# Performance work log

Measured on AMD Instinct MI355X. Metric: run time of the kernel, lower is better.

## Reference

```python
import jax, jax.numpy as jnp
import numpy as np

N_NODES = 100000
N_EDGES = 3200000
N_GRAPHS = 128
IN_DIM = 4
HID = 64
BN_EPS = 1e-5


def setup_inputs() -> dict:
    key = jax.random.key(0)
    ks = jax.random.split(key, 24)
    x = jax.random.normal(ks[0], (N_NODES, IN_DIM), dtype=jnp.float32)
    edge_index = jax.random.randint(ks[1], (2, N_EDGES), 0, N_NODES, dtype=jnp.int32)
    batch_ids = jnp.sort(jax.random.randint(ks[2], (N_NODES,), 0, N_GRAPHS, dtype=jnp.int32))

    def lin(k, out_d, in_d):
        s = 1.0 / np.sqrt(in_d)
        return jax.random.uniform(k, (out_d, in_d), jnp.float32, -s, s)

    inp = {
        'x': x, 'edge_index': edge_index, 'batch_ids': batch_ids,
        # SAGEConv i: out = lin_l(mean_neighbors) + lin_r(x_self); bias lives in lin_l
        'w1l': lin(ks[3], HID, IN_DIM), 'b1': jnp.zeros((HID,), jnp.float32), 'w1r': lin(ks[4], HID, IN_DIM),
        'bn1_g': jnp.ones((HID,), jnp.float32), 'bn1_b': jnp.zeros((HID,), jnp.float32),
        'w2l': lin(ks[5], HID, HID), 'b2': jnp.zeros((HID,), jnp.float32), 'w2r': lin(ks[6], HID, HID),
        'bn2_g': jnp.ones((HID,), jnp.float32), 'bn2_b': jnp.zeros((HID,), jnp.float32),
        'w3l': lin(ks[7], HID, HID), 'b3': jnp.zeros((HID,), jnp.float32), 'w3r': lin(ks[8], HID, HID),
        'bn3_g': jnp.ones((HID,), jnp.float32), 'bn3_b': jnp.zeros((HID,), jnp.float32),
        'fc1_w': lin(ks[9], 64, HID), 'fc1_b': jnp.zeros((64,), jnp.float32),
        'fc2_w': lin(ks[10], 2, 64), 'fc2_b': jnp.zeros((2,), jnp.float32),
    }
    return inp


def _sage(x, src, dst, deg_inv, wl, bl, wr):
    # mean-aggregate neighbor messages (source -> target), then two small GEMMs
    msum = jax.ops.segment_sum(x[src], dst, num_segments=N_NODES)  # [N, d]
    agg = msum * deg_inv[:, None]
    return agg @ wl.T + bl + x @ wr.T


def _bn(x, g, b):
    # BatchNorm1d in training mode: batch stats over node dim, biased variance
    m = jnp.mean(x, axis=0)
    v = jnp.mean((x - m) ** 2, axis=0)
    return (x - m) * jax.lax.rsqrt(v + BN_EPS) * g + b


def reference(x, edge_index, batch_ids,
              w1l, b1, w1r, bn1_g, bn1_b,
              w2l, b2, w2r, bn2_g, bn2_b,
              w3l, b3, w3r, bn3_g, bn3_b,
              fc1_w, fc1_b, fc2_w, fc2_b):
    src, dst = edge_index[0], edge_index[1]
    deg = jax.ops.segment_sum(jnp.ones((src.shape[0],), x.dtype), dst, num_segments=N_NODES)
    deg_inv = 1.0 / jnp.maximum(deg, 1.0)

    h = jax.nn.relu(_bn(_sage(x, src, dst, deg_inv, w1l, b1, w1r), bn1_g, bn1_b))
    h = jax.nn.relu(_bn(_sage(h, src, dst, deg_inv, w2l, b2, w2r), bn2_g, bn2_b))
    h = jax.nn.relu(_bn(_sage(h, src, dst, deg_inv, w3l, b3, w3r), bn3_g, bn3_b))

    # global_mean_pool over graphs
    gsum = jax.ops.segment_sum(h, batch_ids, num_segments=N_GRAPHS)
    gcnt = jax.ops.segment_sum(jnp.ones((h.shape[0],), h.dtype), batch_ids, num_segments=N_GRAPHS)
    pooled = gsum / jnp.maximum(gcnt, 1.0)[:, None]

    # MLP head (dropout = identity at inference)
    hid = jax.nn.relu(pooled @ fc1_w.T + fc1_b)
    return hid @ fc2_w.T + fc2_b
```

## Files before the change

### kernel.cpp

```cpp
#include <hip/hip_runtime.h>
#include <hip/hip_fp16.h>

#define NN 100000
#define NE 3200000
#define NG 128
#define BN_EPS 1e-5f

#define NBUK 782
#define BSHIFT 7
#define BCAP 6144

#define GRID_SG 1024
#define PBMAX 2048
#define PSLICE 8

typedef _Float16 h2v __attribute__((ext_vector_type(2)));
typedef unsigned int u32x2 __attribute__((ext_vector_type(2)));
typedef unsigned int u32x4 __attribute__((ext_vector_type(4)));


__global__ void __launch_bounds__(512) k_scatter(
    const int* __restrict__ src, const int* __restrict__ dst,
    int* __restrict__ slab_cursor, unsigned int* __restrict__ slab, int E) {
    __shared__ int hist[NBUK + 2];
    __shared__ int cbase[NBUK + 2];
    int tid = threadIdx.x;
    int eBeg = blockIdx.x * 6250;
    int eEnd = min(eBeg + 6250, E);

    for (int t = tid; t < NBUK; t += 512) hist[t] = 0;
    __syncthreads();
    for (int e = eBeg + tid; e < eEnd; e += 512) {
        int b = dst[e] >> BSHIFT;
        atomicAdd(&hist[b], 1);
    }
    __syncthreads();
    for (int t = tid; t < NBUK; t += 512) {
        int c = hist[t];
        cbase[t] = (c > 0) ? atomicAdd(&slab_cursor[t], c) : 0;
    }
    __syncthreads();
    for (int t = tid; t < NBUK; t += 512) hist[t] = 0;
    __syncthreads();
    for (int e = eBeg + tid; e < eEnd; e += 512) {
        int d = dst[e];
        int b = d >> BSHIFT;
        int r = atomicAdd(&hist[b], 1);
        int pos = cbase[b] + r;
        if (pos < BCAP) slab[(size_t)b * BCAP + pos] = ((unsigned)src[e] << BSHIFT) | (unsigned)(d & 127);
    }
}

__global__ void __launch_bounds__(512) k_bucket_csr(
    const unsigned int* __restrict__ slab, const int* __restrict__ slab_cursor,
    int* __restrict__ row_ptr,
    float* __restrict__ deg_inv, int* __restrict__ csr_src,
    const float* __restrict__ x, const float* __restrict__ w1l,
    const float* __restrict__ b1, const float* __restrict__ w1r,
    __half* __restrict__ hp16, float* __restrict__ part) {
    __shared__ int lds_csr[BCAP];
    __shared__ int red[512];
    __shared__ int sdeg[128];
    __shared__ int sscan[128];
    __shared__ int slcur[128];
    __shared__ float swl[256], swr[256], sb1[64];
    __shared__ float ssum[64], ssq[64];
    int tid = threadIdx.x;
    int b = blockIdx.x;
    int lo = b << BSHIFT;
    int cnt = min(slab_cursor[b], BCAP);
    const unsigned int* sl = slab + (size_t)b * BCAP;

    int partial = 0;
    for (int j = tid; j < b; j += 512) partial += min(slab_cursor[j], BCAP);
    red[tid] = partial;
    __syncthreads();
    for (int off = 256; off > 0; off >>= 1) {
        if (tid < off) red[tid] += red[tid + off];
        __syncthreads();
    }
    int base = red[0];
    if (b == NBUK - 1 && tid == 0) row_ptr[NN] = base + cnt;

    if (tid < 256) { swl[tid] = w1l[tid]; swr[tid] = w1r[tid]; }
    if (tid < 64)  { sb1[tid] = b1[tid]; ssum[tid] = 0.f; ssq[tid] = 0.f; }
    if (tid < 128) sdeg[tid] = 0;
    __syncthreads();
    for (int k = tid; k < cnt; k += 512) {
        atomicAdd(&sdeg[sl[k] & 127], 1);
    }
    __syncthreads();
    int v = (tid < 128) ? sdeg[tid] : 0;
    if (tid < 128) sscan[tid] = v;
    __syncthreads();
    for (int off = 1; off < 128; off <<= 1) {
        int add = 0;
        if (tid < 128 && tid >= off) add = sscan[tid - off];
        __syncthreads();
        if (tid < 128) sscan[tid] += add;
        __syncthreads();
    }
    if (tid < 128) {
        int excl = sscan[tid] - v;
        int n = lo + tid;
        if (n < NN) {
            row_ptr[n] = base + excl;
            deg_inv[n] = 1.0f / fmaxf((float)v, 1.0f);
        }
        slcur[tid] = excl;
    }
    __syncthreads();
    for (int k = tid; k < cnt; k += 512) {
        unsigned int p = sl[k];
        int pos = atomicAdd(&slcur[p & 127], 1);
        lds_csr[pos] = (int)(p >> BSHIFT);
    }
    __syncthreads();
    for (int k = tid; k < cnt; k += 512) csr_src[base + k] = lds_csr[k];

    int i = tid >> 2, c = tid & 3;
    int n = lo + i;
    bool valid = (n < NN);
    int dhi = sscan[i];
    int dlo = dhi - sdeg[i];
    const float4* x4 = (const float4*)x;
    float4 acc = make_float4(0.f, 0.f, 0.f, 0.f);
    int k = dlo + c;
    for (; k + 12 < dhi; k += 16) {
        int s0 = lds_csr[k], s1 = lds_csr[k + 4], s2 = lds_csr[k + 8], s3 = lds_csr[k + 12];
        float4 v0 = x4[s0];
        float4 v1 = x4[s1];
        float4 v2 = x4[s2];
        float4 v3 = x4[s3];
        acc.x += v0.x + v1.x + v2.x + v3.x;
        acc.y += v0.y + v1.y + v2.y + v3.y;
        acc.z += v0.z + v1.z + v2.z + v3.z;
        acc.w += v0.w + v1.w + v2.w + v3.w;
    }
    for (; k < dhi; k += 4) {
        int s = lds_csr[k];
        float4 xv = x4[s];
        acc.x += xv.x; acc.y += xv.y; acc.z += xv.z; acc.w += xv.w;
    }
#pragma unroll
    for (int m = 1; m <= 2; m <<= 1) {
        acc.x += __shfl_xor(acc.x, m);
        acc.y += __shfl_xor(acc.y, m);
        acc.z += __shfl_xor(acc.z, m);
        acc.w += __shfl_xor(acc.w, m);
    }
    float dv = 1.0f / fmaxf((float)sdeg[i], 1.0f);
    float ax = acc.x * dv, ay = acc.y * dv, az = acc.z * dv, aw = acc.w * dv;
    float4 xs = valid ? x4[n] : make_float4(0.f, 0.f, 0.f, 0.f);

#pragma unroll
    for (int m4 = 0; m4 < 4; m4++) {
        float4 o = make_float4(0.f, 0.f, 0.f, 0.f);
        float* op = &o.x;
        if (valid) {
#pragma unroll
            for (int t = 0; t < 4; t++) {
                int j = c * 16 + m4 * 4 + t;
                float s = sb1[j];
                s += ax * swl[j * 4 + 0] + ay * swl[j * 4 + 1] + az * swl[j * 4 + 2] + aw * swl[j * 4 + 3];
                s += xs.x * swr[j * 4 + 0] + xs.y * swr[j * 4 + 1] + xs.z * swr[j * 4 + 2] + xs.w * swr[j * 4 + 3];
                op[t] = s;
            }
            h2v p0 = h2v{(_Float16)o.x, (_Float16)o.y};
            h2v p1 = h2v{(_Float16)o.z, (_Float16)o.w};
            u32x2 w;
            w.x = *(unsigned int*)&p0;
            w.y = *(unsigned int*)&p1;
            __builtin_nontemporal_store(w, (u32x2*)hp16 + (size_t)n * 16 + c * 4 + m4);
        }
        float4 q = make_float4(o.x * o.x, o.y * o.y, o.z * o.z, o.w * o.w);
#pragma unroll
        for (int m = 4; m <= 32; m <<= 1) {
            o.x += __shfl_xor(o.x, m); o.y += __shfl_xor(o.y, m);
            o.z += __shfl_xor(o.z, m); o.w += __shfl_xor(o.w, m);
            q.x += __shfl_xor(q.x, m); q.y += __shfl_xor(q.y, m);
            q.z += __shfl_xor(q.z, m); q.w += __shfl_xor(q.w, m);
        }
        if ((tid & 63) < 4) {
            int jb = c * 16 + m4 * 4;
            atomicAdd(&ssum[jb + 0], o.x); atomicAdd(&ssum[jb + 1], o.y);
            atomicAdd(&ssum[jb + 2], o.z); atomicAdd(&ssum[jb + 3], o.w);
            atomicAdd(&ssq[jb + 0], q.x);  atomicAdd(&ssq[jb + 1], q.y);
            atomicAdd(&ssq[jb + 2], q.z);  atomicAdd(&ssq[jb + 3], q.w);
        }
    }
    __syncthreads();
    if (tid < 64) {
        part[(2 * tid) * PBMAX + blockIdx.x]     = ssum[tid];
        part[(2 * tid + 1) * PBMAX + blockIdx.x] = ssq[tid];
    }
}

__global__ void __launch_bounds__(512, 8) k_sage(
    const __half* __restrict__ h_in, const float* __restrict__ sbv_in,
    const int* __restrict__ row_ptr,
    const int* __restrict__ csr_src, const float* __restrict__ deg_inv,
    const float* __restrict__ wl, const float* __restrict__ bl,
    const float* __restrict__ wr, __half* __restrict__ hp16,
    float* __restrict__ part) {
    __shared__ h2v wl2s[32][68];
    __shared__ h2v wr2s[32][68];
    __shared__ h2v tAh[32][36];
    __shared__ h2v tXh[32][36];
    __shared__ float ssum[64], ssq[64];
    int tid = threadIdx.x;
    for (int idx = tid; idx < 2048; idx += 512) {
        int j = idx & 63, kk = idx >> 6;
        float2 l = ((const float2*)wl)[j * 32 + kk];
        float2 r = ((const float2*)wr)[j * 32 + kk];
        wl2s[kk][j] = h2v{(_Float16)l.x, (_Float16)l.y};
        wr2s[kk][j] = h2v{(_Float16)r.x, (_Float16)r.y};
    }
    if (tid < 64) { ssum[tid] = 0.f; ssq[tid] = 0.f; }
    __syncthreads();

    int g = tid & 15, ni = tid >> 4;
    h2v sch0 = h2v{(_Float16)sbv_in[4 * g + 0], (_Float16)sbv_in[4 * g + 1]};
    h2v sch1 = h2v{(_Float16)sbv_in[4 * g + 2], (_Float16)sbv_in[4 * g + 3]};
    h2v bih0 = h2v{(_Float16)sbv_in[64 + 4 * g + 0], (_Float16)sbv_in[64 + 4 * g + 1]};
    h2v bih1 = h2v{(_Float16)sbv_in[64 + 4 * g + 2], (_Float16)sbv_in[64 + 4 * g + 3]};
    h2v hz = h2v{(_Float16)0.f, (_Float16)0.f};

    const uint2* tbl = (const uint2*)h_in;
    const int ntiles = NN / 32;

#define BN_ACC(vv) { \
        h2v a0 = *(h2v*)&vv.x, a1 = *(h2v*)&vv.y; \
        a0 = __builtin_elementwise_max(a0 * sch0 + bih0, hz); \
        a1 = __builtin_elementwise_max(a1 * sch1 + bih1, hz); \
        ax += (float)a0.x; ay += (float)a0.y; az += (float)a1.x; aw += (float)a1.y; }

    for (int tile = blockIdx.x; tile < ntiles; tile += GRID_SG) {
        int n = tile * 32 + ni;
        float ax = 0.f, ay = 0.f, az = 0.f, aw = 0.f;
        int r0 = row_ptr[n], r1 = row_ptr[n + 1];
        int e = r0;
        for (; e + 8 <= r1; e += 8) {
            int s0 = csr_src[e],     s1 = csr_src[e + 1], s2 = csr_src[e + 2], s3 = csr_src[e + 3];
            int s4 = csr_src[e + 4], s5 = csr_src[e + 5], s6 = csr_src[e + 6], s7 = csr_src[e + 7];
            uint2 v0 = tbl[(size_t)s0 * 16 + g];
            uint2 v1 = tbl[(size_t)s1 * 16 + g];
            uint2 v2 = tbl[(size_t)s2 * 16 + g];
            uint2 v3 = tbl[(size_t)s3 * 16 + g];
            uint2 v4 = tbl[(size_t)s4 * 16 + g];
            uint2 v5 = tbl[(size_t)s5 * 16 + g];
            uint2 v6 = tbl[(size_t)s6 * 16 + g];
            uint2 v7 = tbl[(size_t)s7 * 16 + g];
            BN_ACC(v0) BN_ACC(v1) BN_ACC(v2) BN_ACC(v3)
            BN_ACC(v4) BN_ACC(v5) BN_ACC(v6) BN_ACC(v7)
        }
        for (; e < r1; ++e) {
            int s = csr_src[e];
            uint2 vv = tbl[(size_t)s * 16 + g];
            BN_ACC(vv)
        }
        float di = deg_inv[n];
        uint2 rsv = tbl[(size_t)n * 16 + g];
        h2v xs0h = __builtin_elementwise_max(*(h2v*)&rsv.x * sch0 + bih0, hz);
        h2v xs1h = __builtin_elementwise_max(*(h2v*)&rsv.y * sch1 + bih1, hz);
        ax *= di; ay *= di; az *= di; aw *= di;
        tAh[ni][2 * g]     = h2v{(_Float16)ax, (_Float16)ay};
        tAh[ni][2 * g + 1] = h2v{(_Float16)az, (_Float16)aw};
        tXh[ni][2 * g]     = xs0h;
        tXh[ni][2 * g + 1] = xs1h;
        __syncthreads();

        float4 o = ((const float4*)bl)[g];
#pragma unroll 4
        for (int kk = 0; kk < 32; kk++) {
            h2v a2 = tAh[ni][kk];
            h2v x2 = tXh[ni][kk];
            h2v l0 = wl2s[kk][4 * g + 0], l1 = wl2s[kk][4 * g + 1];
            h2v l2 = wl2s[kk][4 * g + 2], l3 = wl2s[kk][4 * g + 3];
            h2v r0v = wr2s[kk][4 * g + 0], r1v = wr2s[kk][4 * g + 1];
            h2v r2v = wr2s[kk][4 * g + 2], r3v = wr2s[kk][4 * g + 3];
#if __has_builtin(__builtin_amdgcn_fdot2)
            o.x = __builtin_amdgcn_fdot2(a2, l0, o.x, false);
            o.y = __builtin_amdgcn_fdot2(a2, l1, o.y, false);
            o.z = __builtin_amdgcn_fdot2(a2, l2, o.z, false);
            o.w = __builtin_amdgcn_fdot2(a2, l3, o.w, false);
            o.x = __builtin_amdgcn_fdot2(x2, r0v, o.x, false);
            o.y = __builtin_amdgcn_fdot2(x2, r1v, o.y, false);
            o.z = __builtin_amdgcn_fdot2(x2, r2v, o.z, false);
            o.w = __builtin_amdgcn_fdot2(x2, r3v, o.w, false);
#else
            float b0 = (float)a2.x, b1 = (float)a2.y, x0 = (float)x2.x, x1 = (float)x2.y;
            o.x += b0 * (float)l0.x + b1 * (float)l0.y + x0 * (float)r0v.x + x1 * (float)r0v.y;
            o.y += b0 * (float)l1.x + b1 * (float)l1.y + x0 * (float)r1v.x + x1 * (float)r1v.y;
            o.z += b0 * (float)l2.x + b1 * (float)l2.y + x0 * (float)r2v.x + x1 * (float)r2v.y;
            o.w += b0 * (float)l3.x + b1 * (float)l3.y + x0 * (float)r3v.x + x1 * (float)r3v.y;
#endif
        }
        {
            h2v p0 = h2v{(_Float16)o.x, (_Float16)o.y};
            h2v p1 = h2v{(_Float16)o.z, (_Float16)o.w};
            u32x2 w;
            w.x = *(unsigned int*)&p0;
            w.y = *(unsigned int*)&p1;
            __builtin_nontemporal_store(w, (u32x2*)hp16 + (size_t)n * 16 + g);
        }

        float4 qv = make_float4(o.x * o.x, o.y * o.y, o.z * o.z, o.w * o.w);
#pragma unroll
        for (int m = 16; m <= 32; m <<= 1) {
            o.x += __shfl_xor(o.x, m); o.y += __shfl_xor(o.y, m);
            o.z += __shfl_xor(o.z, m); o.w += __shfl_xor(o.w, m);
            qv.x += __shfl_xor(qv.x, m); qv.y += __shfl_xor(qv.y, m);
            qv.z += __shfl_xor(qv.z, m); qv.w += __shfl_xor(qv.w, m);
        }
        if ((tid & 48) == 0) {
            atomicAdd(&ssum[4 * g + 0], o.x); atomicAdd(&ssum[4 * g + 1], o.y);
            atomicAdd(&ssum[4 * g + 2], o.z); atomicAdd(&ssum[4 * g + 3], o.w);
            atomicAdd(&ssq[4 * g + 0], qv.x);  atomicAdd(&ssq[4 * g + 1], qv.y);
            atomicAdd(&ssq[4 * g + 2], qv.z);  atomicAdd(&ssq[4 * g + 3], qv.w);
        }
        __syncthreads();
    }
#undef BN_ACC
    if (tid < 64) {
        part[(2 * tid) * PBMAX + blockIdx.x]     = ssum[tid];
        part[(2 * tid + 1) * PBMAX + blockIdx.x] = ssq[tid];
    }
}

__global__ void k_reduce_sb(const float* __restrict__ part, int PB,
                            const float* __restrict__ gamma, const float* __restrict__ beta,
                            float* __restrict__ sbv, int N) {
    int c = blockIdx.x;
    float s = 0.f, q = 0.f;
    for (int b = threadIdx.x; b < PB; b += 256) {
        s += part[(2 * c) * PBMAX + b];
        q += part[(2 * c + 1) * PBMAX + b];
    }
    __shared__ float rs[256], rq[256];
    rs[threadIdx.x] = s;
    rq[threadIdx.x] = q;
    __syncthreads();
    for (int off = 128; off > 0; off >>= 1) {
        if (threadIdx.x < off) {
            rs[threadIdx.x] += rs[threadIdx.x + off];
            rq[threadIdx.x] += rq[threadIdx.x + off];
        }
        __syncthreads();
    }
    if (threadIdx.x == 0) {
        float m = rs[0] / (float)N;
        float var = rq[0] / (float)N - m * m;
        float sc = gamma[c] * rsqrtf(var + BN_EPS);
        sbv[c]      = sc;
        sbv[64 + c] = beta[c] - m * sc;
    }
}

__global__ void __launch_bounds__(256) k_pool_partial(
    const __half* __restrict__ hp16, const float* __restrict__ sbv,
    const int* __restrict__ batch, float* __restrict__ pooled_part, int N) {
    __shared__ float ssc[64], sbi[64];
    __shared__ float sm[256];
    if (threadIdx.x < 64) {
        ssc[threadIdx.x] = sbv[threadIdx.x];
        sbi[threadIdx.x] = sbv[64 + threadIdx.x];
    }
    __syncthreads();
    int gph = blockIdx.x >> 3;
    int slice = blockIdx.x & 7;
    int lo = 0, hi = N;
    while (lo < hi) { int mid = (lo + hi) >> 1; if (batch[mid] < gph) lo = mid + 1; else hi = mid; }
    int start = lo;
    hi = N;
    while (lo < hi) { int mid = (lo + hi) >> 1; if (batch[mid] < gph + 1) lo = mid + 1; else hi = mid; }
    int end = lo;

    int c = threadIdx.x & 63, w = threadIdx.x >> 6;
    float s = 0.f;
    for (int r = start + slice * 4 + w; r < end; r += 32)
        s += fmaxf(__half2float(hp16[(size_t)r * 64 + c]) * ssc[c] + sbi[c], 0.f);
    sm[threadIdx.x] = s;
    __syncthreads();
    if (threadIdx.x < 64) {
        float t = sm[c] + sm[64 + c] + sm[128 + c] + sm[192 + c];
        pooled_part[(size_t)(gph * PSLICE + slice) * 64 + c] = t;
    }
}

__global__ void __launch_bounds__(64) k_head(
    const float* __restrict__ pooled_part, const int* __restrict__ batch,
    const float* __restrict__ fc1w, const float* __restrict__ fc1b,
    const float* __restrict__ fc2w, const float* __restrict__ fc2b,
    float* __restrict__ out, int N) {
    __shared__ float pl[64], hid[64];
    int gph = blockIdx.x;
    int j = threadIdx.x;
    int lo = 0, hi = N;
    while (lo < hi) { int mid = (lo + hi) >> 1; if (batch[mid] < gph) lo = mid + 1; else hi = mid; }
    int start = lo;
    hi = N;
    while (lo < hi) { int mid = (lo + hi) >> 1; if (batch[mid] < gph + 1) lo = mid + 1; else hi = mid; }
    int cnt = lo - start;

    float t = 0.f;
#pragma unroll
    for (int s = 0; s < PSLICE; s++) t += pooled_part[(size_t)(gph * PSLICE + s) * 64 + j];
    pl[j] = t / fmaxf((float)cnt, 1.0f);
    __syncthreads();
    float v = fc1b[j];
    for (int k = 0; k < 64; k++) v += pl[k] * fc1w[j * 64 + k];
    hid[j] = fmaxf(v, 0.f);
    __syncthreads();
    if (j < 2) {
        float o = fc2b[j];
        for (int k = 0; k < 64; k++) o += hid[k] * fc2w[j * 64 + k];
        out[gph * 2 + j] = o;
    }
}

extern "C" void kernel_launch(void* const* d_in, const int* in_sizes, int n_in,
                              void* d_out, int out_size, void* d_ws, size_t ws_size,
                              hipStream_t stream) {
    const float* x    = (const float*)d_in[0];
    const int* ei     = (const int*)d_in[1];
    const int* batch  = (const int*)d_in[2];
    const float* w1l  = (const float*)d_in[3];
    const float* b1   = (const float*)d_in[4];
    const float* w1r  = (const float*)d_in[5];
    const float* bn1g = (const float*)d_in[6];
    const float* bn1b = (const float*)d_in[7];
    const float* w2l  = (const float*)d_in[8];
    const float* b2   = (const float*)d_in[9];
    const float* w2r  = (const float*)d_in[10];
    const float* bn2g = (const float*)d_in[11];
    const float* bn2b = (const float*)d_in[12];
    const float* w3l  = (const float*)d_in[13];
    const float* b3   = (const float*)d_in[14];
    const float* w3r  = (const float*)d_in[15];
    const float* bn3g = (const float*)d_in[16];
    const float* bn3b = (const float*)d_in[17];
    const float* fc1w = (const float*)d_in[18];
    const float* fc1b = (const float*)d_in[19];
    const float* fc2w = (const float*)d_in[20];
    const float* fc2b = (const float*)d_in[21];
    float* out = (float*)d_out;

    const int N = NN, E = NE;
    const int* srcp = ei;
    const int* dstp = ei + E;

    char* ws = (char*)d_ws;
    size_t off = 0;
    auto alloc = [&](size_t bytes) -> char* {
        char* p = ws + off;
        off += (bytes + 255) & ~(size_t)255;
        return p;
    };
    int* csr_src       = (int*)alloc(sizeof(int) * E);
    __half* hpA        = (__half*)alloc(sizeof(__half) * N * 64);
    __half* hpB        = (__half*)alloc(sizeof(__half) * N * 64);
    unsigned int* slab = (unsigned int*)alloc(sizeof(unsigned int) * (size_t)NBUK * BCAP);
    int* slab_cursor   = (int*)alloc(sizeof(int) * NBUK);
    int* row_ptr       = (int*)alloc(sizeof(int) * (N + 1));
    float* deg_inv     = (float*)alloc(sizeof(float) * N);
    float* part        = (float*)alloc(sizeof(float) * 128 * PBMAX);
    float* sbv         = (float*)alloc(sizeof(float) * 128);
    float* pooled_part = (float*)alloc(sizeof(float) * NG * PSLICE * 64);

    hipMemsetAsync(slab_cursor, 0, sizeof(int) * NBUK, stream);

    k_scatter<<<512, 512, 0, stream>>>(srcp, dstp, slab_cursor, slab, E);
    k_bucket_csr<<<NBUK, 512, 0, stream>>>(slab, slab_cursor, row_ptr, deg_inv,
                                           csr_src, x, w1l, b1, w1r, hpA, part);
    k_reduce_sb<<<64, 256, 0, stream>>>(part, NBUK, bn1g, bn1b, sbv, N);

    k_sage<<<GRID_SG, 512, 0, stream>>>(hpA, sbv, row_ptr, csr_src, deg_inv,
                                        w2l, b2, w2r, hpB, part);
    k_reduce_sb<<<64, 256, 0, stream>>>(part, GRID_SG, bn2g, bn2b, sbv, N);

    k_sage<<<GRID_SG, 512, 0, stream>>>(hpB, sbv, row_ptr, csr_src, deg_inv,
                                        w3l, b3, w3r, hpA, part);
    k_reduce_sb<<<64, 256, 0, stream>>>(part, GRID_SG, bn3g, bn3b, sbv, N);

    k_pool_partial<<<NG * PSLICE, 256, 0, stream>>>(hpA, sbv, batch, pooled_part, N);
    k_head<<<NG, 64, 0, stream>>>(pooled_part, batch, fc1w, fc1b, fc2w, fc2b, out, N);
}
```

Baseline: 394.4 us.

## Accumulate neighbor sums in fp16 per chunk, cache slab entries in registers, halve scatter grid

The SAGE gather loop now sums each batch of 8 neighbors in packed fp16 before converting to fp32, which cuts conversions and adds. The bucket CSR kernel loads each slab entry into registers once and reuses it for both the degree count and the placement pass, so the slab is read once instead of twice. The scatter kernel runs half as many blocks, each covering twice as many edges, which means fewer global cursor atomics. The fp16 partial sums lose some precision, and the register array is fixed at 12 entries, which silently drops edges if a bucket holds more than 12×512 of them.

```diff
diff --git a/kernel.cpp b/kernel.cpp
--- a/kernel.cpp
+++ b/kernel.cpp
@@ -25,8 +25,8 @@
     __shared__ int hist[NBUK + 2];
     __shared__ int cbase[NBUK + 2];
     int tid = threadIdx.x;
-    int eBeg = blockIdx.x * 6250;
-    int eEnd = min(eBeg + 6250, E);
+    int eBeg = blockIdx.x * 12500;
+    int eEnd = min(eBeg + 12500, E);
 
     for (int t = tid; t < NBUK; t += 512) hist[t] = 0;
     __syncthreads();
@@ -86,9 +86,13 @@
     if (tid < 64)  { sb1[tid] = b1[tid]; ssum[tid] = 0.f; ssq[tid] = 0.f; }
     if (tid < 128) sdeg[tid] = 0;
     __syncthreads();
-    for (int k = tid; k < cnt; k += 512) {
-        atomicAdd(&sdeg[sl[k] & 127], 1);
-    }
+
+    unsigned int myv[12];
+    int mycount = 0;
+    for (int k = tid; k < cnt; k += 512) myv[mycount++] = sl[k];
+#pragma unroll
+    for (int j = 0; j < 12; j++)
+        if (j < mycount) atomicAdd(&sdeg[myv[j] & 127], 1);
     __syncthreads();
     int v = (tid < 128) ? sdeg[tid] : 0;
     if (tid < 128) sscan[tid] = v;
@@ -110,11 +114,13 @@
         slcur[tid] = excl;
     }
     __syncthreads();
-    for (int k = tid; k < cnt; k += 512) {
-        unsigned int p = sl[k];
-        int pos = atomicAdd(&slcur[p & 127], 1);
-        lds_csr[pos] = (int)(p >> BSHIFT);
-    }
+#pragma unroll
+    for (int j = 0; j < 12; j++)
+        if (j < mycount) {
+            unsigned int p = myv[j];
+            int pos = atomicAdd(&slcur[p & 127], 1);
+            lds_csr[pos] = (int)(p >> BSHIFT);
+        }
     __syncthreads();
     for (int k = tid; k < cnt; k += 512) csr_src[base + k] = lds_csr[k];
 
@@ -229,11 +235,10 @@
     const uint2* tbl = (const uint2*)h_in;
     const int ntiles = NN / 32;
 
-#define BN_ACC(vv) { \
+#define BN_ACC_H(vv) { \
         h2v a0 = *(h2v*)&vv.x, a1 = *(h2v*)&vv.y; \
-        a0 = __builtin_elementwise_max(a0 * sch0 + bih0, hz); \
-        a1 = __builtin_elementwise_max(a1 * sch1 + bih1, hz); \
-        ax += (float)a0.x; ay += (float)a0.y; az += (float)a1.x; aw += (float)a1.y; }
+        hacc0 += __builtin_elementwise_max(a0 * sch0 + bih0, hz); \
+        hacc1 += __builtin_elementwise_max(a1 * sch1 + bih1, hz); }
 
     for (int tile = blockIdx.x; tile < ntiles; tile += GRID_SG) {
         int n = tile * 32 + ni;
@@ -251,13 +256,19 @@
             uint2 v5 = tbl[(size_t)s5 * 16 + g];
             uint2 v6 = tbl[(size_t)s6 * 16 + g];
             uint2 v7 = tbl[(size_t)s7 * 16 + g];
-            BN_ACC(v0) BN_ACC(v1) BN_ACC(v2) BN_ACC(v3)
-            BN_ACC(v4) BN_ACC(v5) BN_ACC(v6) BN_ACC(v7)
+            h2v hacc0 = hz, hacc1 = hz;
+            BN_ACC_H(v0) BN_ACC_H(v1) BN_ACC_H(v2) BN_ACC_H(v3)
+            BN_ACC_H(v4) BN_ACC_H(v5) BN_ACC_H(v6) BN_ACC_H(v7)
+            ax += (float)hacc0.x; ay += (float)hacc0.y;
+            az += (float)hacc1.x; aw += (float)hacc1.y;
         }
         for (; e < r1; ++e) {
             int s = csr_src[e];
             uint2 vv = tbl[(size_t)s * 16 + g];
-            BN_ACC(vv)
+            h2v a0 = *(h2v*)&vv.x, a1 = *(h2v*)&vv.y;
+            a0 = __builtin_elementwise_max(a0 * sch0 + bih0, hz);
+            a1 = __builtin_elementwise_max(a1 * sch1 + bih1, hz);
+            ax += (float)a0.x; ay += (float)a0.y; az += (float)a1.x; aw += (float)a1.y;
         }
         float di = deg_inv[n];
         uint2 rsv = tbl[(size_t)n * 16 + g];
@@ -321,7 +332,7 @@
         }
         __syncthreads();
     }
-#undef BN_ACC
+#undef BN_ACC_H
     if (tid < 64) {
         part[(2 * tid) * PBMAX + blockIdx.x]     = ssum[tid];
         part[(2 * tid + 1) * PBMAX + blockIdx.x] = ssq[tid];
@@ -470,7 +481,7 @@
 
     hipMemsetAsync(slab_cursor, 0, sizeof(int) * NBUK, stream);
 
-    k_scatter<<<512, 512, 0, stream>>>(srcp, dstp, slab_cursor, slab, E);
+    k_scatter<<<256, 512, 0, stream>>>(srcp, dstp, slab_cursor, slab, E);
     k_bucket_csr<<<NBUK, 512, 0, stream>>>(slab, slab_cursor, row_ptr, deg_inv,
                                            csr_src, x, w1l, b1, w1r, hpA, part);
     k_reduce_sb<<<64, 256, 0, stream>>>(part, NBUK, bn1g, bn1b, sbv, N);
```

Measured after the change: 377.1 us, median of 2. 1.05x faster.
